# Performance work log

Hardware: AMD Instinct MI355X
Metric: run time of the kernel (lower is better)

## Reference

```python
import jax, jax.numpy as jnp
import numpy as np

K = 5          # top_k periods
KERNEL = 25    # moving-average kernel for series decomposition
D = 64         # d_model / channels
EPS = 1e-5     # BatchNorm eps (torch default)


def setup_inputs() -> dict:
    key = jax.random.key(0)
    k0, k1, k2, k3, k4 = jax.random.split(key, 5)
    B, T = 8, 2048
    x = jax.random.normal(k0, (B, T, D), jnp.float32)
    w1 = jax.random.normal(k1, (D, D, 3, 3), jnp.float32) * 0.05
    w2 = jax.random.normal(k2, (D, D, 3, 3), jnp.float32) * 0.05
    bn1_gamma = jnp.ones((D,), jnp.float32) + 0.1 * jax.random.normal(k3, (D,), jnp.float32)
    bn2_gamma = jnp.ones((D,), jnp.float32) + 0.1 * jax.random.normal(k4, (D,), jnp.float32)
    z = jnp.zeros((D,), jnp.float32)
    o = jnp.ones((D,), jnp.float32)
    return dict(x=x, w1=w1, w2=w2,
                bn1_gamma=bn1_gamma, bn1_beta=z, bn1_mean=z, bn1_var=o,
                bn2_gamma=bn2_gamma, bn2_beta=z, bn2_mean=z, bn2_var=o)


def _moving_avg(x, kernel):
    # AvgPool1d(stride=1, padding=(kernel-1)//2, count_include_pad=False) over time.
    T = x.shape[1]
    pad = (kernel - 1) // 2
    cs = jnp.concatenate([jnp.zeros_like(x[:, :1]), jnp.cumsum(x, axis=1)], axis=1)  # [B,T+1,C]
    t = jnp.arange(T)
    lo = jnp.clip(t - pad, 0, T)          # inclusive window start
    hi = jnp.clip(t + pad + 1, 0, T)      # exclusive window end
    sums = cs[:, hi] - cs[:, lo]
    return sums / (hi - lo).astype(x.dtype)[None, :, None]


def _auto_corr(s, k):
    T = s.shape[1]
    Xf = jnp.fft.rfft(s, axis=1)
    Pm = (Xf * jnp.conj(Xf)).real.mean(axis=-1)          # [B, T//2+1]
    r = jnp.fft.irfft(Pm, n=T, axis=1)                   # [B, T]
    r = r.at[:, 0].set(-jnp.inf)                          # forbid lag 0
    vals, idx = jax.lax.top_k(r, k)                       # [B,k]
    w = jax.nn.softmax(vals, axis=1)
    return idx, w


def _bn(z, gamma, beta, mean, var):
    return (z - mean) * (gamma * jax.lax.rsqrt(var + EPS)) + beta


def _process_one(s_b, p, w1, w2, bn1, bn2):
    # s_b: [T, C]; p: scalar int period.
    # Equivalent to: roll(s_b, -p), reflect-pad time to cyc*p, fold to [C,cyc,p],
    # Conv2dResBlock (3x3 zero-pad convs + eval BN + GELU + residual), unfold, crop to T.
    T, C = s_b.shape
    U = 2 * T - 2                               # static bound: cyc*p <= T+p-1 <= 2T-2
    u = jnp.arange(U)
    cyc = (T + p - 1) // p
    v = jnp.where(u < T, u, 2 * T - 2 - u)      # reflect extension index
    g = s_b[(v + p) % T]                         # [U,C] rolled-by-(-p) then reflect-padded
    r = u // p                                   # grid row (cycle)
    c = u % p                                    # grid col (phase)

    def conv3x3(z, w):
        # zero-padded 3x3 conv on the [cyc, p] grid, expressed on the flat time axis
        out = jnp.zeros_like(z)
        for dr in (-1, 0, 1):
            for dc in (-1, 0, 1):
                valid = (r + dr >= 0) & (r + dr < cyc) & (c + dc >= 0) & (c + dc < p)
                un = jnp.clip(u + dr * p + dc, 0, U - 1)
                zn = jnp.where(valid[:, None], z[un], 0.0)    # [U,C]
                out = out + zn @ w[:, :, dr + 1, dc + 1].T    # [U,Cout]
        return out

    h = _bn(conv3x3(g, w1), *bn1)
    h = jax.nn.gelu(h, approximate=False)
    h = _bn(conv3x3(h, w2), *bn2)
    return (g + h)[:T]                           # residual + unfold-crop


def reference(x, w1, w2, bn1_gamma, bn1_beta, bn1_mean, bn1_var,
              bn2_gamma, bn2_beta, bn2_mean, bn2_var):
    trend = _moving_avg(x, KERNEL)
    s = x - trend                                # seasonal
    idx, w = _auto_corr(s, K)                    # [B,K] periods, weights
    bn1 = (bn1_gamma, bn1_beta, bn1_mean, bn1_var)
    bn2 = (bn2_gamma, bn2_beta, bn2_mean, bn2_var)
    f = lambda sb, p: _process_one(sb, p, w1, w2, bn1, bn2)
    y = jax.vmap(lambda sb, pb: jax.vmap(lambda p: f(sb, p))(pb))(s, idx)  # [B,K,T,C]
    agg = jnp.einsum('bk,bktc->btc', w, y)
    return agg + trend + x
```

## Files before the change

kernel.cpp:

```cpp
#include <hip/hip_runtime.h>
#include <hip/hip_bf16.h>
#include <math.h>

#define TB 8
#define TT 2048
#define TD 64
#define TK 5
#define TPAD 12
#define EPSBN 1e-5f
#define UMAX 4096

#define ROWS 64
#define BAND 66
#define LROWS 198

#define ROWS2 16
#define BAND2 18
#define LROWS2 54
#define SH8   432
#define BUFB  6912

typedef __attribute__((ext_vector_type(8))) short short8;
typedef __attribute__((ext_vector_type(4))) float f32x4;

#define OFF_S     0
#define OFF_SBF   1048576
#define OFF_R     1572864
#define OFF_IDX   1581056
#define OFF_W     1581096
#define OFF_WT1   1581136
#define OFF_WT2   1599568
#define OFF_H1    1618000

__global__ __launch_bounds__(256) void k_trend(const float* __restrict__ x,
                                               float* __restrict__ out, float* __restrict__ s,
                                               __hip_bfloat16* __restrict__ sbf,
                                               const float* __restrict__ w1, const float* __restrict__ w2,
                                               __hip_bfloat16* __restrict__ wt1, __hip_bfloat16* __restrict__ wt2,
                                               float* __restrict__ r)
{
    if (blockIdx.x >= 256) {
        int d = (blockIdx.x - 256) * 256 + threadIdx.x;
        if (d < TB * 1024) r[d] = 0.f;
        if (d < 36864) {
            int j = d & 7, l = (d >> 3) & 63, nt = (d >> 9) & 3, kb = d >> 11;
            int tap = kb >> 1, half = kb & 1;
            int co = nt * 16 + (l & 15);
            int ci = half * 32 + (l >> 4) * 8 + j;
            int src = (co * 64 + ci) * 9 + tap;
            wt1[d] = __float2bfloat16(w1[src]);
            wt2[d] = __float2bfloat16(w2[src]);
        }
        return;
    }
    int gid = blockIdx.x * 256 + threadIdx.x;
    int c = gid & 63;
    int tblk = (gid >> 6) & 127;
    int b = gid >> 13;
    int t0 = tblk * 16;
    const float* base = x + (size_t)b * TT * TD + c;
    float sum = 0.f;
    for (int tt = t0 - TPAD; tt <= t0 + TPAD; ++tt)
        if (tt >= 0 && tt < TT) sum += base[(size_t)tt * TD];
    size_t o = (size_t)b * TT * TD + (size_t)t0 * TD + c;
    #pragma unroll
    for (int i = 0; i < 16; ++i) {
        int t = t0 + i;
        int lo = t - TPAD; if (lo < 0) lo = 0;
        int hi = t + TPAD; if (hi > TT - 1) hi = TT - 1;
        float tr = sum / (float)(hi - lo + 1);
        float xv = base[(size_t)t * TD];
        out[o] = xv + tr;
        float sv = xv - tr;
        s[o] = sv;
        sbf[o] = __float2bfloat16(sv);
        int addt = t + TPAD + 1, subt = t - TPAD;
        if (addt < TT) sum += base[(size_t)addt * TD];
        if (subt >= 0) sum -= base[(size_t)subt * TD];
        o += TD;
    }
}

__global__ __launch_bounds__(256) void k_autocorr(const float* __restrict__ s, float* __restrict__ r)
{
    int b = blockIdx.z;
    int l0 = blockIdx.x * 16 + 1;
    const float* sb = s + (size_t)b * TT * TD;
    int cg = (threadIdx.x & 15) * 4;
    int tg = threadIdx.x >> 4;
    int t0 = blockIdx.y * 1024 + tg * 64;
    const int RB = TD * 4;
    const int TTB = TT * TD * 4;
    float acc[16];
    #pragma unroll
    for (int j = 0; j < 16; ++j) acc[j] = 0.f;
    float4 win[16];
    int wi = t0 + l0; if (wi >= TT) wi -= TT;
    int woff = wi * RB + cg * 4;
    int aoff = t0 * RB + cg * 4;
    #pragma unroll
    for (int m = 0; m < 16; ++m) {
        win[m] = *(const float4*)((const char*)sb + woff);
        woff += RB; if (woff >= TTB) woff -= TTB;
    }
    float4 a_pf = *(const float4*)((const char*)sb + aoff);
    aoff += RB;
    for (int it = 0; it < 4; ++it) {
        #pragma unroll
        for (int jj = 0; jj < 16; ++jj) {
            float4 a = a_pf;
            a_pf = *(const float4*)((const char*)sb + aoff);
            aoff += RB;
            #pragma unroll
            for (int j = 0; j < 16; ++j) {
                float4 w = win[(jj + j) & 15];
                acc[j] = fmaf(a.x, w.x, acc[j]);
                acc[j] = fmaf(a.y, w.y, acc[j]);
                acc[j] = fmaf(a.z, w.z, acc[j]);
                acc[j] = fmaf(a.w, w.w, acc[j]);
            }
            win[jj] = *(const float4*)((const char*)sb + woff);
            woff += RB; if (woff >= TTB) woff -= TTB;
        }
    }
    __shared__ float red[16 * 256];
    #pragma unroll
    for (int j = 0; j < 16; ++j) red[j * 256 + threadIdx.x] = acc[j];
    __syncthreads();
    int j = threadIdx.x >> 4, i = threadIdx.x & 15;
    float v = 0.f;
    #pragma unroll
    for (int m = 0; m < 16; ++m) v += red[j * 256 + i + 16 * m];
    #pragma unroll
    for (int mask = 8; mask; mask >>= 1) v += __shfl_xor(v, mask);
    if (i == 0) atomicAdd(&r[(size_t)b * 1024 + (l0 - 1 + j)], v * (1.0f / 64.0f));
}

__global__ __launch_bounds__(256) void k_topk(const float* __restrict__ r,
                                              int* __restrict__ selidx, float* __restrict__ selw)
{
    int b = blockIdx.x;
    __shared__ float v[1024];
    __shared__ float redv[256]; __shared__ int redi[256];
    __shared__ int s_idx[6]; __shared__ float s_val[6]; __shared__ int slots;
    for (int i = threadIdx.x; i < 1024; i += 256) v[i] = r[(size_t)b * 1024 + i];
    if (threadIdx.x == 0) slots = 0;
    __syncthreads();
    for (int round = 0; round < 5; ++round) {
        if (slots >= 5) break;
        float bv = -INFINITY; int bi = 1 << 30;
        for (int i = threadIdx.x; i < 1024; i += 256) {
            float val = v[i];
            if (val > bv) { bv = val; bi = i; }
        }
        redv[threadIdx.x] = bv; redi[threadIdx.x] = bi;
        __syncthreads();
        for (int off = 128; off; off >>= 1) {
            if (threadIdx.x < off) {
                float ov = redv[threadIdx.x + off]; int oi = redi[threadIdx.x + off];
                float mv = redv[threadIdx.x];       int mi = redi[threadIdx.x];
                if (ov > mv || (ov == mv && oi < mi)) { redv[threadIdx.x] = ov; redi[threadIdx.x] = oi; }
            }
            __syncthreads();
        }
        if (threadIdx.x == 0) {
            int lag = redi[0] + 1; float val = redv[0];
            s_idx[slots] = lag; s_val[slots] = val; slots++;
            if (slots < 5 && lag < 1024) { s_idx[slots] = 2048 - lag; s_val[slots] = val; slots++; }
            v[lag - 1] = -INFINITY;
        }
        __syncthreads();
    }
    if (threadIdx.x == 0) {
        float mx = -INFINITY;
        for (int i = 0; i < 5; ++i) mx = fmaxf(mx, s_val[i]);
        float e[5], sum = 0.f;
        for (int i = 0; i < 5; ++i) { e[i] = expf(s_val[i] - mx); sum += e[i]; }
        for (int i = 0; i < 5; ++i) { selidx[b * TK + i] = s_idx[i]; selw[b * TK + i] = e[i] / sum; }
    }
}

__global__ __launch_bounds__(256) void k_mm1(
    const short* __restrict__ s_bf, const short* __restrict__ wtp,
    const float* __restrict__ g1, const float* __restrict__ b1,
    const float* __restrict__ m1, const float* __restrict__ v1,
    const int* __restrict__ sel, __hip_bfloat16* __restrict__ h1)
{
    int b = blockIdx.z, k = blockIdx.y;
    int p = sel[b * TK + k];
    int cyc = (TT + p - 1) / p;
    int U = cyc * p;
    int u0 = blockIdx.x * ROWS;
    if (u0 >= U) return;
    __shared__ short As[LROWS * 64];

    const short* sb = s_bf + (size_t)b * TT * TD;
    for (int q = threadIdx.x; q < LROWS * 8; q += 256) {
        int row = q >> 3, ch = (q & 7) * 8;
        int band = row / BAND, i = row - band * BAND;
        int w = u0 + (band - 1) * p - 1 + i;
        int wc = min(max(w, 0), 2 * TT - 2);
        int v = (wc < TT) ? wc : (2 * TT - 2 - wc);
        int sr = (v + p) & (TT - 1);
        short8 d = *(const short8*)(sb + (size_t)sr * TD + ch);
        int off = (row * 128 + ch * 2) ^ ((row & 7) << 4);
        *(short8*)((char*)As + off) = d;
    }
    __syncthreads();

    int lane = threadIdx.x & 63;
    int wv = threadIdx.x >> 6;
    int lr = lane & 15;
    int kg = lane >> 4;
    int lu = wv * 16 + lr;
    int u = u0 + lu;
    bool inU = (u < U);
    int r = u / p, c = u - r * p;
    bool topf = (r == 0), botf = (r == cyc - 1), leftf = (c == 0), rightf = (c == p - 1);

    f32x4 acc[4] = {};
    short8 zero = {};
    #pragma unroll
    for (int kb = 0; kb < 18; ++kb) {
        const int tap = kb >> 1, half = kb & 1;
        const int dr = tap / 3 - 1, dc = tap % 3 - 1;
        int ldsrow = (dr + 1) * BAND + lu + 1 + dc;
        int off = (ldsrow * 128 + half * 64 + kg * 16) ^ ((ldsrow & 7) << 4);
        short8 a = *(const short8*)((const char*)As + off);
        bool valid = inU
                   && !(dr == -1 && topf) && !(dr == 1 && botf)
                   && !(dc == -1 && leftf) && !(dc == 1 && rightf);
        if (!valid) a = zero;
        #pragma unroll
        for (int nt = 0; nt < 4; ++nt) {
            short8 bq = *(const short8*)(wtp + (size_t)(kb * 4 + nt) * 512 + lane * 8);
            acc[nt] = __builtin_amdgcn_mfma_f32_16x16x32_bf16(a, bq, acc[nt], 0, 0, 0);
        }
    }
    __hip_bfloat16* ho = h1 + (size_t)(b * TK + k) * (UMAX * TD);
    #pragma unroll
    for (int nt = 0; nt < 4; ++nt) {
        int co = nt * 16 + lr;
        float scale = g1[co] * rsqrtf(v1[co] + EPSBN);
        float bias = b1[co] - m1[co] * scale;
        #pragma unroll
        for (int q = 0; q < 4; ++q) {
            int uo = u0 + wv * 16 + kg * 4 + q;
            if (uo < U) {
                float z = acc[nt][q] * scale + bias;
                float ge = 0.5f * z * (1.0f + erff(z * 0.70710678118654752f));
                ho[(size_t)uo * TD + co] = __float2bfloat16(ge);
            }
        }
    }
}

__global__ __launch_bounds__(256) void k_mm2f(
    const short* __restrict__ h1, const short* __restrict__ wtp,
    const float* __restrict__ s,
    const float* __restrict__ g2, const float* __restrict__ b2,
    const float* __restrict__ m2, const float* __restrict__ v2,
    const int* __restrict__ sel, const float* __restrict__ selw,
    float* __restrict__ out)
{
    int b = blockIdx.y;
    int u0 = blockIdx.x * ROWS2;
    int tid = threadIdx.x;
    __shared__ short As[2 * LROWS2 * 64];

    int lane = tid & 63, wv = tid >> 6, lr = lane & 15, kg = lane >> 4;
    int u = u0 + lr;
    const float* sb = s + (size_t)b * TT * TD;

    f32x4 accT = {};
    float gacc[4] = {0.f, 0.f, 0.f, 0.f};
    short8 sreg[2];
    short8 zero = {};

    {
        int p0 = sel[b * TK];
        const short* hb = h1 + (size_t)(b * TK) * (UMAX * TD);
        #pragma unroll
        for (int it = 0; it < 2; ++it) {
            int q = tid + it * 256;
            if (q < SH8) {
                int row = q >> 3, ch = (q & 7) * 8;
                int band = row / BAND2, i = row - band * BAND2;
                int w = u0 + (band - 1) * p0 - 1 + i;
                int wc = min(max(w, 0), UMAX - 1);
                short8 d = *(const short8*)(hb + (size_t)wc * TD + ch);
                int off = (row * 128 + ch * 2) ^ ((row & 7) << 4);
                *(short8*)((char*)As + off) = d;
            }
        }
    }
    __syncthreads();

    for (int k = 0; k < TK; ++k) {
        int p = sel[b * TK + k];
        float wk = selw[b * TK + k];
        int cyc = (TT + p - 1) / p;
        if (k < TK - 1) {
            int pn = sel[b * TK + k + 1];
            const short* hb = h1 + (size_t)(b * TK + k + 1) * (UMAX * TD);
            #pragma unroll
            for (int it = 0; it < 2; ++it) {
                int q = tid + it * 256;
                if (q < SH8) {
                    int row = q >> 3, ch = (q & 7) * 8;
                    int band = row / BAND2, i = row - band * BAND2;
                    int w = u0 + (band - 1) * pn - 1 + i;
                    int wc = min(max(w, 0), UMAX - 1);
                    sreg[it] = *(const short8*)(hb + (size_t)wc * TD + ch);
                }
            }
        }
        const char* Ab = (const char*)As + (k & 1) * BUFB;
        int r = u / p, c = u - r * p;
        bool topf = (r == 0), botf = (r == cyc - 1), leftf = (c == 0), rightf = (c == p - 1);
        f32x4 accP[2] = {};
        #pragma unroll
        for (int kb = 0; kb < 18; ++kb) {
            const int tap = kb >> 1, half = kb & 1;
            const int dr = tap / 3 - 1, dc = tap % 3 - 1;
            int ldsrow = (dr + 1) * BAND2 + lr + 1 + dc;
            int off = (ldsrow * 128 + half * 64 + kg * 16) ^ ((ldsrow & 7) << 4);
            short8 a = *(const short8*)(Ab + off);
            bool valid = !(dr == -1 && topf) && !(dr == 1 && botf)
                       && !(dc == -1 && leftf) && !(dc == 1 && rightf);
            if (!valid) a = zero;
            short8 bq = *(const short8*)(wtp + (size_t)(kb * 4 + wv) * 512 + lane * 8);
            accP[kb & 1] = __builtin_amdgcn_mfma_f32_16x16x32_bf16(a, bq, accP[kb & 1], 0, 0, 0);
        }
        #pragma unroll
        for (int e = 0; e < 4; ++e) accT[e] += wk * (accP[0][e] + accP[1][e]);
        #pragma unroll
        for (int q = 0; q < 4; ++q) {
            int uo = u0 + kg * 4 + q;
            int sr = (uo + p) & (TT - 1);
            gacc[q] = fmaf(wk, sb[(size_t)sr * TD + wv * 16 + lr], gacc[q]);
        }
        __syncthreads();
        if (k < TK - 1) {
            char* Aw = (char*)As + ((k + 1) & 1) * BUFB;
            #pragma unroll
            for (int it = 0; it < 2; ++it) {
                int q = tid + it * 256;
                if (q < SH8) {
                    int row = q >> 3, ch = (q & 7) * 8;
                    int off = (row * 128 + ch * 2) ^ ((row & 7) << 4);
                    *(short8*)(Aw + off) = sreg[it];
                }
            }
            __syncthreads();
        }
    }

    float* ob = out + (size_t)b * TT * TD;
    int co = wv * 16 + lr;
    float scale = g2[co] * rsqrtf(v2[co] + EPSBN);
    float bias = b2[co] - m2[co] * scale;
    #pragma unroll
    for (int q = 0; q < 4; ++q) {
        int uo = u0 + kg * 4 + q;
        size_t idx = (size_t)uo * TD + co;
        ob[idx] = ob[idx] + gacc[q] + scale * accT[q] + bias;
    }
}

extern "C" void kernel_launch(void* const* d_in, const int* in_sizes, int n_in,
                              void* d_out, int out_size, void* d_ws, size_t ws_size,
                              hipStream_t stream)
{
    const float* x  = (const float*)d_in[0];
    const float* w1 = (const float*)d_in[1];
    const float* w2 = (const float*)d_in[2];
    const float* g1 = (const float*)d_in[3];
    const float* b1 = (const float*)d_in[4];
    const float* m1 = (const float*)d_in[5];
    const float* v1 = (const float*)d_in[6];
    const float* g2 = (const float*)d_in[7];
    const float* b2 = (const float*)d_in[8];
    const float* m2 = (const float*)d_in[9];
    const float* v2 = (const float*)d_in[10];

    float* ws    = (float*)d_ws;
    float* s     = ws + OFF_S;
    __hip_bfloat16* sbf = (__hip_bfloat16*)(ws + OFF_SBF);
    float* r     = ws + OFF_R;
    int*   sel   = (int*)(ws + OFF_IDX);
    float* selw  = ws + OFF_W;
    __hip_bfloat16* wt1 = (__hip_bfloat16*)(ws + OFF_WT1);
    __hip_bfloat16* wt2 = (__hip_bfloat16*)(ws + OFF_WT2);
    __hip_bfloat16* h1  = (__hip_bfloat16*)(ws + OFF_H1);
    float* out   = (float*)d_out;

    k_trend   <<<dim3(400),         dim3(256), 0, stream>>>(x, out, s, sbf, w1, w2, wt1, wt2, r);
    k_autocorr<<<dim3(64, 2, TB),   dim3(256), 0, stream>>>(s, r);
    k_topk    <<<dim3(TB),          dim3(256), 0, stream>>>(r, sel, selw);
    k_mm1     <<<dim3(64, TK, TB),  dim3(256), 0, stream>>>((const short*)sbf, (const short*)wt1,
                                                            g1, b1, m1, v1, sel, h1);
    k_mm2f    <<<dim3(128, TB),     dim3(256), 0, stream>>>((const short*)h1, (const short*)wt2, s,
                                                            g2, b2, m2, v2, sel, selw, out);
}
```

Baseline: 119.8 us.

## Fuse top-k into autocorrelation via last-block counter and split time range further

Removes the separate top-k kernel launch: each autocorrelation block atomically increments a per-batch counter after adding its partial sums, and the last block to finish for a batch runs the top-k and softmax selection, reusing the shared reduction buffer. The time range is also split into four chunks instead of two, which doubles the grid and halves the work per block for more parallelism. This saves a launch and its gap, at the cost of more atomics to the correlation array and a serialized tail in the last block per batch.

```diff
diff --git a/kernel.cpp b/kernel.cpp
--- a/kernel.cpp
+++ b/kernel.cpp
@@ -19,6 +19,8 @@
 #define LROWS2 54
 #define SH8   432
 #define BUFB  6912
+
+#define AC_NBLK 256
 
 typedef __attribute__((ext_vector_type(8))) short short8;
 typedef __attribute__((ext_vector_type(4))) float f32x4;
@@ -31,17 +33,19 @@
 #define OFF_WT1   1581136
 #define OFF_WT2   1599568
 #define OFF_H1    1618000
+#define OFF_CNT   6860880
 
 __global__ __launch_bounds__(256) void k_trend(const float* __restrict__ x,
                                                float* __restrict__ out, float* __restrict__ s,
                                                __hip_bfloat16* __restrict__ sbf,
                                                const float* __restrict__ w1, const float* __restrict__ w2,
                                                __hip_bfloat16* __restrict__ wt1, __hip_bfloat16* __restrict__ wt2,
-                                               float* __restrict__ r)
+                                               float* __restrict__ r, int* __restrict__ cnt)
 {
     if (blockIdx.x >= 256) {
         int d = (blockIdx.x - 256) * 256 + threadIdx.x;
         if (d < TB * 1024) r[d] = 0.f;
+        if (d < TB) cnt[d] = 0;
         if (d < 36864) {
             int j = d & 7, l = (d >> 3) & 63, nt = (d >> 9) & 3, kb = d >> 11;
             int tap = kb >> 1, half = kb & 1;
@@ -81,14 +85,16 @@
     }
 }
 
-__global__ __launch_bounds__(256) void k_autocorr(const float* __restrict__ s, float* __restrict__ r)
+__global__ __launch_bounds__(256) void k_autocorr(const float* __restrict__ s, float* __restrict__ r,
+                                                  int* __restrict__ cnt,
+                                                  int* __restrict__ selidx, float* __restrict__ selw)
 {
     int b = blockIdx.z;
     int l0 = blockIdx.x * 16 + 1;
     const float* sb = s + (size_t)b * TT * TD;
     int cg = (threadIdx.x & 15) * 4;
     int tg = threadIdx.x >> 4;
-    int t0 = blockIdx.y * 1024 + tg * 64;
+    int t0 = blockIdx.y * 512 + tg * 32;
     const int RB = TD * 4;
     const int TTB = TT * TD * 4;
     float acc[16];
@@ -105,7 +111,7 @@
     }
     float4 a_pf = *(const float4*)((const char*)sb + aoff);
     aoff += RB;
-    for (int it = 0; it < 4; ++it) {
+    for (int it = 0; it < 2; ++it) {
         #pragma unroll
         for (int jj = 0; jj < 16; ++jj) {
             float4 a = a_pf;
@@ -127,23 +133,31 @@
     #pragma unroll
     for (int j = 0; j < 16; ++j) red[j * 256 + threadIdx.x] = acc[j];
     __syncthreads();
-    int j = threadIdx.x >> 4, i = threadIdx.x & 15;
-    float v = 0.f;
-    #pragma unroll
-    for (int m = 0; m < 16; ++m) v += red[j * 256 + i + 16 * m];
-    #pragma unroll
-    for (int mask = 8; mask; mask >>= 1) v += __shfl_xor(v, mask);
-    if (i == 0) atomicAdd(&r[(size_t)b * 1024 + (l0 - 1 + j)], v * (1.0f / 64.0f));
-}
-
-__global__ __launch_bounds__(256) void k_topk(const float* __restrict__ r,
-                                              int* __restrict__ selidx, float* __restrict__ selw)
-{
-    int b = blockIdx.x;
-    __shared__ float v[1024];
-    __shared__ float redv[256]; __shared__ int redi[256];
+    {
+        int j = threadIdx.x >> 4, i = threadIdx.x & 15;
+        float v = 0.f;
+        #pragma unroll
+        for (int m = 0; m < 16; ++m) v += red[j * 256 + i + 16 * m];
+        #pragma unroll
+        for (int mask = 8; mask; mask >>= 1) v += __shfl_xor(v, mask);
+        if (i == 0) atomicAdd(&r[(size_t)b * 1024 + (l0 - 1 + j)], v * (1.0f / 64.0f));
+    }
+    __threadfence();
+    __syncthreads();
+    __shared__ int lastFlag;
+    if (threadIdx.x == 0) {
+        int prev = __hip_atomic_fetch_add(&cnt[b], 1, __ATOMIC_ACQ_REL, __HIP_MEMORY_SCOPE_AGENT);
+        lastFlag = (prev == AC_NBLK - 1);
+    }
+    __syncthreads();
+    if (!lastFlag) return;
+
+    float* v    = red;
+    float* redv = red + 1024;
+    int*   redi = (int*)(red + 1280);
     __shared__ int s_idx[6]; __shared__ float s_val[6]; __shared__ int slots;
-    for (int i = threadIdx.x; i < 1024; i += 256) v[i] = r[(size_t)b * 1024 + i];
+    for (int i = threadIdx.x; i < 1024; i += 256)
+        v[i] = __hip_atomic_load(&r[(size_t)b * 1024 + i], __ATOMIC_RELAXED, __HIP_MEMORY_SCOPE_AGENT);
     if (threadIdx.x == 0) slots = 0;
     __syncthreads();
     for (int round = 0; round < 5; ++round) {
@@ -393,11 +407,11 @@
     __hip_bfloat16* wt1 = (__hip_bfloat16*)(ws + OFF_WT1);
     __hip_bfloat16* wt2 = (__hip_bfloat16*)(ws + OFF_WT2);
     __hip_bfloat16* h1  = (__hip_bfloat16*)(ws + OFF_H1);
+    int*   cnt   = (int*)(ws + OFF_CNT);
     float* out   = (float*)d_out;
 
-    k_trend   <<<dim3(400),         dim3(256), 0, stream>>>(x, out, s, sbf, w1, w2, wt1, wt2, r);
-    k_autocorr<<<dim3(64, 2, TB),   dim3(256), 0, stream>>>(s, r);
-    k_topk    <<<dim3(TB),          dim3(256), 0, stream>>>(r, sel, selw);
+    k_trend   <<<dim3(400),         dim3(256), 0, stream>>>(x, out, s, sbf, w1, w2, wt1, wt2, r, cnt);
+    k_autocorr<<<dim3(64, 4, TB),   dim3(256), 0, stream>>>(s, r, cnt, sel, selw);
     k_mm1     <<<dim3(64, TK, TB),  dim3(256), 0, stream>>>((const short*)sbf, (const short*)wt1,
                                                             g1, b1, m1, v1, sel, h1);
     k_mm2f    <<<dim3(128, TB),     dim3(256), 0, stream>>>((const short*)h1, (const short*)wt2, s,
```

Result: slower. 278.9 us (+132.7%).
